# Performance work log

Measured on AMD Instinct MI355X. Metric: run time of the kernel, lower is better.

## Reference

```python
import jax, jax.numpy as jnp
import numpy as np

B, T, K, H = 8, 1024, 512, 8


def setup_inputs() -> dict:
    key = jax.random.key(0)
    kx, kq, kk, kv, ko = jax.random.split(key, 5)
    s = 0.02
    return {
        "x": jax.random.normal(kx, (B, T, K), dtype=jnp.float32),
        "Wq": jax.random.normal(kq, (K * H, K), dtype=jnp.float32) * s,
        "Wk": jax.random.normal(kk, (K * H, K), dtype=jnp.float32) * s,
        "Wv": jax.random.normal(kv, (K * H, K), dtype=jnp.float32) * s,
        "Wo": jax.random.normal(ko, (K, K * H), dtype=jnp.float32) * s,
    }


def reference(x, Wq, Wk, Wv, Wo):
    b, t, k = x.shape
    h = H
    scale = k ** 0.25  # applied to both q and k, total 1/sqrt(k)
    # torch Linear: y = x @ W.T ; view (b,t,h,k) then move heads out: (b,h,t,k)
    def proj(W):
        return (x @ W.T).reshape(b, t, h, k).transpose(0, 2, 1, 3)
    q = proj(Wq) / scale
    kk_ = proj(Wk) / scale
    v = proj(Wv)
    dot = jnp.einsum("bhtd,bhsd->bhts", q, kk_)  # (b,h,t,t)
    # causal mask: strict upper triangle (j > i) -> -inf
    causal = jnp.tril(jnp.ones((t, t), dtype=bool))
    dot = jnp.where(causal[None, None], dot, -jnp.inf)
    attn = jax.nn.softmax(dot, axis=-1)
    out = jnp.einsum("bhts,bhsd->bhtd", attn, v)  # (b,h,t,k)
    out = out.transpose(0, 2, 1, 3).reshape(b, t, h * k)
    return out @ Wo.T
```

## Files before the change

### kernel.cpp

```cpp
#include <hip/hip_runtime.h>
#include <hip/hip_bf16.h>
#include <cstdint>
#include <cmath>


typedef __attribute__((ext_vector_type(8))) short short8;
typedef __attribute__((ext_vector_type(4))) float f32x4;

#define DEVINL __device__ __forceinline__

DEVINL float bf2f(ushort u) { union { uint32_t i; float f; } w; w.i = (uint32_t)u << 16; return w.f; }
DEVINL ushort f2bf(float f) {
  union { float f; uint32_t i; } w; w.f = f;
  uint32_t r = w.i + 0x7FFFu + ((w.i >> 16) & 1u);
  return (ushort)(r >> 16);
}

DEVINL void gl_lds16(const ushort* g, ushort* l) {
  __builtin_amdgcn_global_load_lds(
      (const __attribute__((address_space(1))) uint32_t*)g,
      (__attribute__((address_space(3))) uint32_t*)l, 16, 0, 0);
}

__global__ __launch_bounds__(256) void cvt_f32_bf16(const float* __restrict__ in,
                                                    ushort* __restrict__ out,
                                                    int n8, float scale) {
  int i = blockIdx.x * 256 + threadIdx.x;
  if (i >= n8) return;
  const float4* p = (const float4*)in + (size_t)i * 2;
  float4 a = p[0], b = p[1];
  short8 o;
  o[0] = (short)f2bf(a.x * scale); o[1] = (short)f2bf(a.y * scale);
  o[2] = (short)f2bf(a.z * scale); o[3] = (short)f2bf(a.w * scale);
  o[4] = (short)f2bf(b.x * scale); o[5] = (short)f2bf(b.y * scale);
  o[6] = (short)f2bf(b.z * scale); o[7] = (short)f2bf(b.w * scale);
  ((short8*)out)[i] = o;
}

__global__ __launch_bounds__(256) void zerof4(float4* __restrict__ p, int n4) {
  int i = blockIdx.x * 256 + threadIdx.x;
  if (i < n4) p[i] = float4{0.f, 0.f, 0.f, 0.f};
}

template<bool CSKIP, bool CKB, int EPI, bool ZBH>
__global__ __launch_bounds__(512, 2) void gemm256(
    const ushort* __restrict__ A0, long long sAb, long long sAh,
    const ushort* __restrict__ B0, long long sBb, long long sBh,
    void* __restrict__ C0, long long sCb, long long sCh,
    int lda, int ldb, int ldc, int K)
{
  const int bm = blockIdx.x, bn = blockIdx.y, bz = blockIdx.z;
  if (CSKIP && bn > bm) return;
  long long za, zb, zc;
  if (ZBH) {
    const long long bi = bz >> 3, hi = bz & 7;
    za = bi * sAb + hi * sAh; zb = bi * sBb + hi * sBh; zc = bi * sCb + hi * sCh;
  } else {
    za = (long long)bz * sAh; zb = (long long)bz * sBh; zc = (long long)bz * sCh;
  }
  const ushort* A = A0 + za;
  const ushort* B = B0 + zb;
  int kend = K;
  if (CKB) { int kb = (bm + 1) * 256; kend = kb < K ? kb : K; }

  __shared__ ushort smem[65536];

  const int tid = threadIdx.x;
  const int wid = tid >> 6, lane = tid & 63;
  const int wr = wid >> 2, wc = wid & 3;
  const int l15 = lane & 15, kq = lane >> 4;

  const int srow8 = lane >> 3;
  const int schunk = ((lane & 7) ^ srow8) * 8;
  const ushort* ag = A + (size_t)(bm * 256 + wid * 8 + srow8) * lda + schunk;
  const ushort* bg = B + (size_t)(bn * 256 + wid * 8 + srow8) * ldb + schunk;

  auto STA = [&](int buf, int band, int kk) {
    gl_lds16(ag + (size_t)band * 64 * lda + kk, &smem[buf * 32768 + band * 4096 + wid * 512]);
  };
  auto STB = [&](int buf, int band, int kk) {
    gl_lds16(bg + (size_t)band * 64 * ldb + kk, &smem[buf * 32768 + 16384 + band * 4096 + wid * 512]);
  };
  auto STAGE2 = [&](int buf, int p, int kk) {
    switch (p) {
      case 0: STB(buf, 0, kk); STB(buf, 1, kk); break;
      case 1: STB(buf, 2, kk); STB(buf, 3, kk); break;
      case 2: STA(buf, 0, kk); STA(buf, 2, kk); break;
      default: STA(buf, 1, kk); STA(buf, 3, kk); break;
    }
  };

  f32x4 acc[8][4] = {};
  const int nt = kend >> 6;

#pragma unroll
  for (int p = 0; p < 4; ++p) STAGE2(0, p, 0);

  short8 bq[4];
  for (int t = 0; t < nt; ++t) {
    const int cur = t & 1;
    const ushort* As = &smem[cur * 32768];
    const ushort* Bs = As + 16384;
    const bool pre = (t + 1 < nt);
    const int kk1 = (t + 1) << 6;

#pragma unroll
    for (int ph = 0; ph < 4; ++ph) {
      const int mh = ph & 1, ks = ph >> 1;
      if (pre) STAGE2(cur ^ 1, ph, kk1);
      if (ph == 0) {
        if (pre) asm volatile("s_waitcnt vmcnt(4)" ::: "memory");
        else     asm volatile("s_waitcnt vmcnt(2)" ::: "memory");
        __builtin_amdgcn_sched_barrier(0);
        __builtin_amdgcn_s_barrier();
        __builtin_amdgcn_sched_barrier(0);
      } else if (ph == 1) {
        if (pre) asm volatile("s_waitcnt vmcnt(4)" ::: "memory");
        else     asm volatile("s_waitcnt vmcnt(0)" ::: "memory");
        __builtin_amdgcn_sched_barrier(0);
        __builtin_amdgcn_s_barrier();
        __builtin_amdgcn_sched_barrier(0);
      }

      if (mh == 0) {
#pragma unroll
        for (int n = 0; n < 4; ++n)
          bq[n] = *(const short8*)
              &Bs[(wc * 64 + n * 16 + l15) * 64 + (((ks * 4 + kq) ^ (l15 & 7)) * 8)];
      }
      short8 av[4];
#pragma unroll
      for (int m = 0; m < 4; ++m)
        av[m] = *(const short8*)
            &As[(wr * 128 + mh * 64 + m * 16 + l15) * 64 + (((ks * 4 + kq) ^ (l15 & 7)) * 8)];

      __builtin_amdgcn_s_setprio(1);
#pragma unroll
      for (int m = 0; m < 4; ++m)
#pragma unroll
        for (int n = 0; n < 4; ++n)
          acc[mh * 4 + m][n] =
              __builtin_amdgcn_mfma_f32_16x16x32_bf16(av[m], bq[n], acc[mh * 4 + m][n], 0, 0, 0);
      __builtin_amdgcn_s_setprio(0);

      if (ph == 3) {
        asm volatile("s_waitcnt lgkmcnt(0)" ::: "memory");
        __builtin_amdgcn_sched_barrier(0);
        __builtin_amdgcn_s_barrier();
        __builtin_amdgcn_sched_barrier(0);
      }
    }
  }

  if constexpr (EPI == 0) {
#pragma unroll
    for (int m = 0; m < 8; ++m)
#pragma unroll
      for (int n = 0; n < 4; ++n)
#pragma unroll
        for (int r = 0; r < 4; ++r) {
          const int row = wr * 128 + m * 16 + kq * 4 + r;
          const int col = wc * 64 + n * 16 + l15;
          smem[row * 256 + (((col >> 3) ^ (row & 31)) * 8) + (col & 7)] = f2bf(acc[m][n][r]);
        }
    __syncthreads();
    ushort* C = (ushort*)C0 + zc;
#pragma unroll
    for (int j = 0; j < 16; ++j) {
      const int chi = j * 512 + tid;
      const int row = chi >> 5, cc = chi & 31;
      *(short8*)&C[(size_t)(bm * 256 + row) * ldc + bn * 256 + cc * 8] =
          *(const short8*)&smem[row * 256 + ((cc ^ (row & 31)) * 8)];
    }
  } else {
    float* C = (float*)C0 + zc;
#pragma unroll
    for (int m = 0; m < 8; ++m)
#pragma unroll
      for (int n = 0; n < 4; ++n)
#pragma unroll
        for (int r = 0; r < 4; ++r)
          atomicAdd(&C[(size_t)(bm * 256 + wr * 128 + m * 16 + kq * 4 + r) * ldc
                       + bn * 256 + wc * 64 + n * 16 + l15], acc[m][n][r]);
  }
}

__global__ __launch_bounds__(256) void transposeV(const ushort* __restrict__ QKVg,
                                                  ushort* __restrict__ Vtg) {
  __shared__ ushort tile[64][72];
  const int bx = blockIdx.x;
  const int by = blockIdx.y;
  const int bz = blockIdx.z;
  const int b = bz >> 3, h = bz & 7;
  const int t = threadIdx.x;
  const int r = t >> 2, c = (t & 3) * 16;

  const ushort* src = QKVg + (size_t)(b * 1024 + bx * 64 + r) * 12288 + 8192 + h * 512 + by * 64 + c;
  short8 v0 = *(const short8*)src;
  short8 v1 = *(const short8*)(src + 8);
#pragma unroll
  for (int j = 0; j < 8; ++j) { tile[r][c + j] = (ushort)v0[j]; tile[r][c + 8 + j] = (ushort)v1[j]; }
  __syncthreads();

  ushort* dst = Vtg + (size_t)(bz * 512 + by * 64 + r) * 1024 + bx * 64 + c;
  short8 o0, o1;
#pragma unroll
  for (int j = 0; j < 8; ++j) { o0[j] = (short)tile[c + j][r]; o1[j] = (short)tile[c + 8 + j][r]; }
  *(short8*)dst = o0;
  *(short8*)(dst + 8) = o1;
}

__global__ __launch_bounds__(256) void softmax_causal(ushort* __restrict__ S) {
  const int wave = threadIdx.x >> 6, lane = threadIdx.x & 63;
  const size_t row_id = (size_t)blockIdx.x * 4 + wave;
  const int t = (int)(row_id & 1023);
  ushort* row = S + row_id * 1024;
  const int j0 = lane * 16;

  short8 v0 = *(const short8*)&row[j0];
  short8 v1 = *(const short8*)&row[j0 + 8];
  float f[16];
#pragma unroll
  for (int i = 0; i < 8; ++i) { f[i] = bf2f((ushort)v0[i]); f[8 + i] = bf2f((ushort)v1[i]); }

  float m = -1e30f;
#pragma unroll
  for (int i = 0; i < 16; ++i) {
    if (j0 + i > t) f[i] = -1e30f;
    m = fmaxf(m, f[i]);
  }
#pragma unroll
  for (int off = 32; off; off >>= 1) m = fmaxf(m, __shfl_xor(m, off));

  float s = 0.f;
#pragma unroll
  for (int i = 0; i < 16; ++i) { f[i] = __expf(f[i] - m); s += f[i]; }
#pragma unroll
  for (int off = 32; off; off >>= 1) s += __shfl_xor(s, off);
  const float inv = 1.f / s;

#pragma unroll
  for (int i = 0; i < 8; ++i) {
    v0[i] = (short)f2bf(f[i] * inv);
    v1[i] = (short)f2bf(f[8 + i] * inv);
  }
  *(short8*)&row[j0] = v0;
  *(short8*)&row[j0 + 8] = v1;
}

extern "C" void kernel_launch(void* const* d_in, const int* in_sizes, int n_in,
                              void* d_out, int out_size, void* d_ws, size_t ws_size,
                              hipStream_t stream) {
  const float* x  = (const float*)d_in[0];
  const float* Wq = (const float*)d_in[1];
  const float* Wk = (const float*)d_in[2];
  const float* Wv = (const float*)d_in[3];
  const float* Wo = (const float*)d_in[4];
  float* out = (float*)d_out;

  const int g = (ws_size >= 293601280ull) ? 4 : (ws_size >= 192937984ull) ? 2 : 1;
  const int ng = 8 / g;

  ushort* xb   = (ushort*)d_ws;
  ushort* Wqkv = xb   + (size_t)4194304;
  ushort* Wob  = Wqkv + (size_t)6291456;
  ushort* AO   = Wob  + (size_t)2097152;
  ushort* QKVg = AO   + (size_t)33554432;
  ushort* Vtg  = QKVg + (size_t)g * 12582912;
  ushort* Sg   = Vtg  + (size_t)g * 4194304;

  const float iscale = (float)(1.0 / pow(512.0, 0.25));

  cvt_f32_bf16<<<2048, 256, 0, stream>>>(x,  xb,             524288, 1.0f);
  cvt_f32_bf16<<<1024, 256, 0, stream>>>(Wq, Wqkv,           262144, iscale);
  cvt_f32_bf16<<<1024, 256, 0, stream>>>(Wk, Wqkv + 2097152, 262144, iscale);
  cvt_f32_bf16<<<1024, 256, 0, stream>>>(Wv, Wqkv + 4194304, 262144, 1.0f);
  cvt_f32_bf16<<<1024, 256, 0, stream>>>(Wo, Wob,            262144, 1.0f);

  for (int grp = 0; grp < ng; ++grp) {
    gemm256<false, false, 0, false><<<dim3(g * 4, 48, 1), 512, 0, stream>>>(
        xb + (size_t)grp * g * 524288, 0, 0,
        Wqkv, 0, 0,
        QKVg, 0, 0,
        512, 512, 12288, 512);

    transposeV<<<dim3(16, 8, 8 * g), 256, 0, stream>>>(QKVg, Vtg);

    gemm256<true, false, 0, true><<<dim3(4, 4, 8 * g), 512, 0, stream>>>(
        QKVg,        12582912LL, 512LL,
        QKVg + 4096, 12582912LL, 512LL,
        Sg,          8388608LL,  1048576LL,
        12288, 12288, 1024, 512);

    softmax_causal<<<g * 2048, 256, 0, stream>>>(Sg);

    gemm256<false, true, 0, true><<<dim3(4, 2, 8 * g), 512, 0, stream>>>(
        Sg,  8388608LL, 1048576LL,
        Vtg, 4194304LL, 524288LL,
        AO + (size_t)grp * g * 4194304, 4194304LL, 512LL,
        1024, 1024, 4096, 1024);
  }

  zerof4<<<4096, 256, 0, stream>>>((float4*)out, 1048576);
  gemm256<false, false, 2, false><<<dim3(32, 2, 4), 512, 0, stream>>>(
      AO,  0, 1024LL,
      Wob, 0, 1024LL,
      out, 0, 0LL,
      4096, 4096, 512, 1024);
}
```

Before: 558.7 us.

## Issue all next-tile loads upfront and swizzle block order for XCD locality

The main loop now issues all eight global-to-LDS loads for the next K tile at once, instead of spreading them across four compute phases. The waitcnt thresholds and barriers are adjusted to match, and the compute phases keep the same load-then-MFMA structure. A new SWZ template flag remaps block ids so consecutive tiles land on the same XCD (an 8-way interleave), and it is enabled only for the QKV projection GEMM. The intent is deeper memory overlap and better L2 reuse, at the cost of a burstier issue pattern and possibly less interleaving of memory and MFMA work.

```diff
diff --git a/kernel.cpp b/kernel.cpp
--- a/kernel.cpp
+++ b/kernel.cpp
@@ -42,14 +42,24 @@
   if (i < n4) p[i] = float4{0.f, 0.f, 0.f, 0.f};
 }
 
-template<bool CSKIP, bool CKB, int EPI, bool ZBH>
+template<bool CSKIP, bool CKB, int EPI, bool ZBH, bool SWZ>
 __global__ __launch_bounds__(512, 2) void gemm256(
     const ushort* __restrict__ A0, long long sAb, long long sAh,
     const ushort* __restrict__ B0, long long sBb, long long sBh,
     void* __restrict__ C0, long long sCb, long long sCh,
     int lda, int ldb, int ldc, int K)
 {
-  const int bm = blockIdx.x, bn = blockIdx.y, bz = blockIdx.z;
+  int bm, bn;
+  if (SWZ) {
+    const int X = gridDim.x, nwg = X * gridDim.y;
+    const int bid = blockIdx.y * X + blockIdx.x;
+    const int cpx = nwg >> 3;
+    const int swz = (bid & 7) * cpx + (bid >> 3);
+    bm = swz % X; bn = swz / X;
+  } else {
+    bm = blockIdx.x; bn = blockIdx.y;
+  }
+  const int bz = blockIdx.z;
   if (CSKIP && bn > bm) return;
   long long za, zb, zc;
   if (ZBH) {
@@ -81,59 +91,36 @@
   auto STB = [&](int buf, int band, int kk) {
     gl_lds16(bg + (size_t)band * 64 * ldb + kk, &smem[buf * 32768 + 16384 + band * 4096 + wid * 512]);
   };
-  auto STAGE2 = [&](int buf, int p, int kk) {
-    switch (p) {
-      case 0: STB(buf, 0, kk); STB(buf, 1, kk); break;
-      case 1: STB(buf, 2, kk); STB(buf, 3, kk); break;
-      case 2: STA(buf, 0, kk); STA(buf, 2, kk); break;
-      default: STA(buf, 1, kk); STA(buf, 3, kk); break;
-    }
+  auto STAGE8 = [&](int buf, int kk) {
+    STB(buf, 0, kk); STB(buf, 1, kk); STB(buf, 2, kk); STB(buf, 3, kk);
+    STA(buf, 0, kk); STA(buf, 2, kk); STA(buf, 1, kk); STA(buf, 3, kk);
   };
 
   f32x4 acc[8][4] = {};
   const int nt = kend >> 6;
 
-#pragma unroll
-  for (int p = 0; p < 4; ++p) STAGE2(0, p, 0);
-
-  short8 bq[4];
+  STAGE8(0, 0);
+
   for (int t = 0; t < nt; ++t) {
     const int cur = t & 1;
     const ushort* As = &smem[cur * 32768];
     const ushort* Bs = As + 16384;
     const bool pre = (t + 1 < nt);
-    const int kk1 = (t + 1) << 6;
-
-#pragma unroll
-    for (int ph = 0; ph < 4; ++ph) {
-      const int mh = ph & 1, ks = ph >> 1;
-      if (pre) STAGE2(cur ^ 1, ph, kk1);
-      if (ph == 0) {
-        if (pre) asm volatile("s_waitcnt vmcnt(4)" ::: "memory");
-        else     asm volatile("s_waitcnt vmcnt(2)" ::: "memory");
-        __builtin_amdgcn_sched_barrier(0);
-        __builtin_amdgcn_s_barrier();
-        __builtin_amdgcn_sched_barrier(0);
-      } else if (ph == 1) {
-        if (pre) asm volatile("s_waitcnt vmcnt(4)" ::: "memory");
-        else     asm volatile("s_waitcnt vmcnt(0)" ::: "memory");
-        __builtin_amdgcn_sched_barrier(0);
-        __builtin_amdgcn_s_barrier();
-        __builtin_amdgcn_sched_barrier(0);
-      }
-
-      if (mh == 0) {
-#pragma unroll
-        for (int n = 0; n < 4; ++n)
-          bq[n] = *(const short8*)
-              &Bs[(wc * 64 + n * 16 + l15) * 64 + (((ks * 4 + kq) ^ (l15 & 7)) * 8)];
-      }
-      short8 av[4];
+
+    short8 bq[4], av[4];
+    auto LDB = [&](int ks) {
+#pragma unroll
+      for (int n = 0; n < 4; ++n)
+        bq[n] = *(const short8*)
+            &Bs[(wc * 64 + n * 16 + l15) * 64 + (((ks * 4 + kq) ^ (l15 & 7)) * 8)];
+    };
+    auto LDA = [&](int mh, int ks) {
 #pragma unroll
       for (int m = 0; m < 4; ++m)
         av[m] = *(const short8*)
             &As[(wr * 128 + mh * 64 + m * 16 + l15) * 64 + (((ks * 4 + kq) ^ (l15 & 7)) * 8)];
-
+    };
+    auto MFMAQ = [&](int mh) {
       __builtin_amdgcn_s_setprio(1);
 #pragma unroll
       for (int m = 0; m < 4; ++m)
@@ -142,14 +129,33 @@
           acc[mh * 4 + m][n] =
               __builtin_amdgcn_mfma_f32_16x16x32_bf16(av[m], bq[n], acc[mh * 4 + m][n], 0, 0, 0);
       __builtin_amdgcn_s_setprio(0);
-
-      if (ph == 3) {
-        asm volatile("s_waitcnt lgkmcnt(0)" ::: "memory");
-        __builtin_amdgcn_sched_barrier(0);
-        __builtin_amdgcn_s_barrier();
-        __builtin_amdgcn_sched_barrier(0);
-      }
+    };
+
+    if (pre) {
+      STAGE8(cur ^ 1, (t + 1) << 6);
+      asm volatile("s_waitcnt vmcnt(10)" ::: "memory");
+    } else {
+      asm volatile("s_waitcnt vmcnt(2)" ::: "memory");
     }
+    __builtin_amdgcn_sched_barrier(0);
+    __builtin_amdgcn_s_barrier();
+    __builtin_amdgcn_sched_barrier(0);
+    LDB(0); LDA(0, 0); MFMAQ(0);
+
+    if (pre) asm volatile("s_waitcnt vmcnt(8)" ::: "memory");
+    else     asm volatile("s_waitcnt vmcnt(0)" ::: "memory");
+    __builtin_amdgcn_sched_barrier(0);
+    __builtin_amdgcn_s_barrier();
+    __builtin_amdgcn_sched_barrier(0);
+    LDA(1, 0); MFMAQ(1);
+
+    LDB(1); LDA(0, 1); MFMAQ(0);
+
+    LDA(1, 1); MFMAQ(1);
+    asm volatile("s_waitcnt lgkmcnt(0)" ::: "memory");
+    __builtin_amdgcn_sched_barrier(0);
+    __builtin_amdgcn_s_barrier();
+    __builtin_amdgcn_sched_barrier(0);
   }
 
   if constexpr (EPI == 0) {
@@ -278,7 +284,7 @@
   cvt_f32_bf16<<<1024, 256, 0, stream>>>(Wo, Wob,            262144, 1.0f);
 
   for (int grp = 0; grp < ng; ++grp) {
-    gemm256<false, false, 0, false><<<dim3(g * 4, 48, 1), 512, 0, stream>>>(
+    gemm256<false, false, 0, false, true><<<dim3(g * 4, 48, 1), 512, 0, stream>>>(
         xb + (size_t)grp * g * 524288, 0, 0,
         Wqkv, 0, 0,
         QKVg, 0, 0,
@@ -286,7 +292,7 @@
 
     transposeV<<<dim3(16, 8, 8 * g), 256, 0, stream>>>(QKVg, Vtg);
 
-    gemm256<true, false, 0, true><<<dim3(4, 4, 8 * g), 512, 0, stream>>>(
+    gemm256<true, false, 0, true, false><<<dim3(4, 4, 8 * g), 512, 0, stream>>>(
         QKVg,        12582912LL, 512LL,
         QKVg + 4096, 12582912LL, 512LL,
         Sg,          8388608LL,  1048576LL,
@@ -294,7 +300,7 @@
 
     softmax_causal<<<g * 2048, 256, 0, stream>>>(Sg);
 
-    gemm256<false, true, 0, true><<<dim3(4, 2, 8 * g), 512, 0, stream>>>(
+    gemm256<false, true, 0, true, false><<<dim3(4, 2, 8 * g), 512, 0, stream>>>(
         Sg,  8388608LL, 1048576LL,
         Vtg, 4194304LL, 524288LL,
         AO + (size_t)grp * g * 4194304, 4194304LL, 512LL,
@@ -302,7 +308,7 @@
   }
 
   zerof4<<<4096, 256, 0, stream>>>((float4*)out, 1048576);
-  gemm256<false, false, 2, false><<<dim3(32, 2, 4), 512, 0, stream>>>(
+  gemm256<false, false, 2, false, false><<<dim3(32, 2, 4), 512, 0, stream>>>(
       AO,  0, 1024LL,
       Wob, 0, 1024LL,
       out, 0, 0LL,
```

After: 598.1 us. 1.07x slower.
